# Optimization experiments

Hardware: AMD Instinct MI355X
Metric: run time of the kernel (lower is better)

Reference implementation:

```python
import jax, jax.numpy as jnp
import numpy as np

H = 1024       # hiddenDim
MAXLEN = 512   # maxLen (encoder length)
VOCAB = 32000  # outDim (global in original source)


def setup_inputs() -> dict:
    key = jax.random.key(0)
    ks = jax.random.split(key, 12)
    s = 1.0 / np.sqrt(H)
    u = lambda k, shape: jax.random.uniform(k, shape, jnp.float32, -s, s)
    return {
        "inputId": jax.random.randint(ks[0], (1,), 0, VOCAB),
        "hidden": jax.random.normal(ks[1], (1, 1, H), jnp.float32),
        "encoderOuts": jax.random.normal(ks[2], (MAXLEN, H), jnp.float32),
        "embed_table": jax.random.normal(ks[3], (VOCAB, H), jnp.float32),
        "attn_w": u(ks[4], (MAXLEN, 2 * H)),
        "attn_b": u(ks[5], (MAXLEN,)),
        "comb_w": u(ks[6], (H, 2 * H)),
        "comb_b": u(ks[7], (H,)),
        "w_ih": u(ks[8], (3 * H, H)),
        "w_hh": u(ks[9], (3 * H, H)),
        "b_ih": u(ks[10], (3 * H,)),
        "b_hh": u(ks[11], (3 * H,)),
    }


def reference(inputId, hidden, encoderOuts, embed_table, attn_w, attn_b,
              comb_w, comb_b, w_ih, w_hh, b_ih, b_hh):
    # embedding + (eval-mode) dropout -> identity
    embed = embed_table[inputId].reshape(1, 1, -1)            # (1,1,H)
    # attention over encoder outputs
    cat = jnp.concatenate([embed[0], hidden[0]], axis=1)      # (1,2H)
    attnWeights = jax.nn.softmax(cat @ attn_w.T + attn_b, axis=1)  # (1,MAXLEN)
    attnApplied = attnWeights @ encoderOuts                   # (1,H) == bmm squeeze
    # combine + relu
    x = jnp.concatenate([embed[0], attnApplied], axis=1)      # (1,2H)
    x = jax.nn.relu(x @ comb_w.T + comb_b)                    # (1,H)
    # single GRU step; original calls self.rnn(out) with NO hidden -> h0 = zeros
    h0 = jnp.zeros_like(x)
    gi = x @ w_ih.T + b_ih                                    # (1,3H)
    gh = h0 @ w_hh.T + b_hh                                   # (1,3H)
    i_r, i_z, i_n = jnp.split(gi, 3, axis=1)
    h_r, h_z, h_n = jnp.split(gh, 3, axis=1)
    r = jax.nn.sigmoid(i_r + h_r)
    z = jax.nn.sigmoid(i_z + h_z)
    n = jnp.tanh(i_n + r * h_n)
    h_new = (1.0 - z) * n + z * h0                            # (1,H)
    out = jax.nn.sigmoid(h_new)[None]                         # (1,1,H)
    return out, h_new[None], attnWeights
```

## Files before the change

kernel.cpp:

```cpp
#include <hip/hip_runtime.h>
#include <hip/hip_bf16.h>

#define H 1024
#define MAXLEN 512

typedef __bf16 bf16x8 __attribute__((ext_vector_type(8)));
typedef __bf16 bf16x4 __attribute__((ext_vector_type(4)));
typedef float  f32x4  __attribute__((ext_vector_type(4)));

__device__ __forceinline__ float wave_reduce_sum(float a) {
    #pragma unroll
    for (int off = 32; off; off >>= 1) a += __shfl_xor(a, off);
    return a;
}
__device__ __forceinline__ float wave_reduce_max(float a) {
    #pragma unroll
    for (int off = 32; off; off >>= 1) a = fmaxf(a, __shfl_xor(a, off));
    return a;
}

#define WS_LOGITS 0
#define WS_X      512
#define WS_Y1     2048
#define WS_GT     4096
#define GT_HALF   (1024 * 512)
#define WS_FLOATS (4096 + 2 * GT_HALF)

__global__ __launch_bounds__(512)
void node1(const int* __restrict__ inputId,
           const float* __restrict__ hidden,
           const float* __restrict__ enc,
           const float* __restrict__ embed_table,
           const float* __restrict__ attn_w,
           const float* __restrict__ attn_b,
           const float* __restrict__ comb_w,
           const float* __restrict__ comb_b,
           float* __restrict__ ws) {
    float* logits = ws + WS_LOGITS;
    float* y1     = ws + WS_Y1;

    __shared__ __bf16 Asm[2][128][64];
    __shared__ __bf16 Bsm[2][64][64];

    const int tid  = threadIdx.x;
    const int lane = tid & 63;
    const int w    = tid >> 6;
    const int b    = blockIdx.x;

    if (b < 128) {
        const int pBase = (b & 7) * 128;
        const int qBase = ((b >> 3) & 7) * 64;
        const int kh    = b >> 6;
        const int kBase = kh * 512;
        float* GtH = ws + WS_GT + (size_t)kh * GT_HALF;

        const int wp = w >> 1;
        const int wq = w & 1;
        const int row16 = tid >> 4, c4 = tid & 15;

        f32x4 acc[2][2];
        #pragma unroll
        for (int m = 0; m < 2; ++m)
            #pragma unroll
            for (int n = 0; n < 2; ++n) acc[m][n] = (f32x4){0.f, 0.f, 0.f, 0.f};

        float4 ra[4], rb[2];
        auto loadChunk = [&](int c) {
            const int k0 = kBase + c * 64;
            #pragma unroll
            for (int i = 0; i < 4; ++i)
                ra[i] = *(const float4*)(comb_w + (size_t)(pBase + row16 + i * 32) * 2048 + 1024 + k0 + c4 * 4);
            #pragma unroll
            for (int i = 0; i < 2; ++i)
                rb[i] = *(const float4*)(enc + (size_t)(qBase + row16 + i * 32) * 1024 + k0 + c4 * 4);
        };
        auto writeChunk = [&](int buf) {
            #pragma unroll
            for (int i = 0; i < 4; ++i) {
                int row = row16 + i * 32;
                int off = ((((c4 >> 1) ^ (row & 7)) << 4) | ((c4 & 1) << 3));
                bf16x4 v;
                v[0] = (__bf16)ra[i].x; v[1] = (__bf16)ra[i].y;
                v[2] = (__bf16)ra[i].z; v[3] = (__bf16)ra[i].w;
                *(bf16x4*)((char*)(&Asm[buf][row][0]) + off) = v;
            }
            #pragma unroll
            for (int i = 0; i < 2; ++i) {
                int row = row16 + i * 32;
                int off = ((((c4 >> 1) ^ (row & 7)) << 4) | ((c4 & 1) << 3));
                bf16x4 v;
                v[0] = (__bf16)rb[i].x; v[1] = (__bf16)rb[i].y;
                v[2] = (__bf16)rb[i].z; v[3] = (__bf16)rb[i].w;
                *(bf16x4*)((char*)(&Bsm[buf][row][0]) + off) = v;
            }
        };

        loadChunk(0);
        writeChunk(0);
        __syncthreads();

        for (int c = 0; c < 8; ++c) {
            const int cur = c & 1;
            if (c < 7) loadChunk(c + 1);
            #pragma unroll
            for (int ks = 0; ks < 2; ++ks) {
                const int slot = ks * 4 + (lane >> 4);
                bf16x8 af[2], bfv[2];
                #pragma unroll
                for (int m = 0; m < 2; ++m) {
                    int row = wp * 32 + m * 16 + (lane & 15);
                    af[m] = *(const bf16x8*)((const char*)(&Asm[cur][row][0]) + ((slot ^ (row & 7)) << 4));
                }
                #pragma unroll
                for (int n = 0; n < 2; ++n) {
                    int row = wq * 32 + n * 16 + (lane & 15);
                    bfv[n] = *(const bf16x8*)((const char*)(&Bsm[cur][row][0]) + ((slot ^ (row & 7)) << 4));
                }
                #pragma unroll
                for (int m = 0; m < 2; ++m)
                    #pragma unroll
                    for (int n = 0; n < 2; ++n)
                        acc[m][n] = __builtin_amdgcn_mfma_f32_16x16x32_bf16(af[m], bfv[n], acc[m][n], 0, 0, 0);
            }
            if (c < 7) writeChunk(cur ^ 1);
            __syncthreads();
        }

        #pragma unroll
        for (int m = 0; m < 2; ++m) {
            int p0 = pBase + wp * 32 + m * 16 + (lane >> 4) * 4;
            #pragma unroll
            for (int n = 0; n < 2; ++n) {
                int q = qBase + wq * 32 + n * 16 + (lane & 15);
                #pragma unroll
                for (int i = 0; i < 4; ++i)
                    GtH[(size_t)(p0 + i) * 512 + q] = acc[m][n][i];
            }
        }
    } else if (b < 192) {
        const float* embed = embed_table + (size_t)inputId[0] * H;
        int row = (b - 128) * 8 + w;
        const float* wrow = attn_w + (size_t)row * (2 * H);
        float acc = 0.f;
        #pragma unroll
        for (int it = 0; it < 8; ++it) {
            int base = it * 256 + lane * 4;
            float4 wv = *(const float4*)(wrow + base);
            float4 cv = (it < 4) ? *(const float4*)(embed + base)
                                 : *(const float4*)(hidden + (base - H));
            acc += wv.x * cv.x + wv.y * cv.y + wv.z * cv.z + wv.w * cv.w;
        }
        acc = wave_reduce_sum(acc);
        if (lane == 0) logits[row] = acc + attn_b[row];
    } else {
        const float* embed = embed_table + (size_t)inputId[0] * H;
        #pragma unroll
        for (int rr = 0; rr < 2; ++rr) {
            int row = (b - 192) * 16 + w * 2 + rr;
            const float* wrow = comb_w + (size_t)row * (2 * H);
            float acc = 0.f;
            #pragma unroll
            for (int it = 0; it < 4; ++it) {
                int base = it * 256 + lane * 4;
                float4 wv = *(const float4*)(wrow + base);
                float4 evv = *(const float4*)(embed + base);
                acc += wv.x * evv.x + wv.y * evv.y + wv.z * evv.z + wv.w * evv.w;
            }
            acc = wave_reduce_sum(acc);
            if (lane == 0) y1[row] = acc + comb_b[row];
        }
    }
}

__global__ __launch_bounds__(256)
void node2(float* __restrict__ ws, float* __restrict__ d_out) {
    const float* logits = ws + WS_LOGITS;
    const float* y1     = ws + WS_Y1;
    const float* Gt0    = ws + WS_GT;
    const float* Gt1    = ws + WS_GT + GT_HALF;
    float* x = ws + WS_X;

    __shared__ float wsm[MAXLEN];
    __shared__ float red[4];
    const int tid = threadIdx.x, lane = tid & 63, wid = tid >> 6;
    const int b = blockIdx.x;

    float l0 = logits[tid], l1 = logits[tid + 256];
    float m = wave_reduce_max(fmaxf(l0, l1));
    if (lane == 0) red[wid] = m;
    __syncthreads();
    m = fmaxf(fmaxf(red[0], red[1]), fmaxf(red[2], red[3]));
    __syncthreads();
    float e0 = expf(l0 - m), e1 = expf(l1 - m);
    float s = wave_reduce_sum(e0 + e1);
    if (lane == 0) red[wid] = s;
    __syncthreads();
    s = red[0] + red[1] + red[2] + red[3];
    float inv = 1.f / s;
    float w0 = e0 * inv, w1 = e1 * inv;
    wsm[tid] = w0;
    wsm[tid + 256] = w1;
    if (b == 0) {
        d_out[2048 + tid] = w0;
        d_out[2048 + 256 + tid] = w1;
    }
    __syncthreads();

    #pragma unroll
    for (int rr = 0; rr < 2; ++rr) {
        int row = b * 8 + wid * 2 + rr;
        const float* g0 = Gt0 + (size_t)row * 512;
        const float* g1 = Gt1 + (size_t)row * 512;
        float acc = 0.f;
        #pragma unroll
        for (int i = 0; i < 8; ++i) {
            int k = lane + 64 * i;
            acc += (g0[k] + g1[k]) * wsm[k];
        }
        acc = wave_reduce_sum(acc);
        if (lane == 0) x[row] = fmaxf(y1[row] + acc, 0.f);
    }
}

__global__ __launch_bounds__(256)
void node3(const float* __restrict__ w_ih,
           const float* __restrict__ b_ih,
           const float* __restrict__ b_hh,
           const float* __restrict__ ws,
           float* __restrict__ d_out) {
    const float* x = ws + WS_X;
    int lane = threadIdx.x & 63;
    int j = blockIdx.x * 4 + (threadIdx.x >> 6);
    float acc0 = 0.f, acc1 = 0.f, acc2 = 0.f;
    const float* wr = w_ih + (size_t)j * H;
    const float* wz = w_ih + (size_t)(H + j) * H;
    const float* wn = w_ih + (size_t)(2 * H + j) * H;
    #pragma unroll
    for (int it = 0; it < 4; ++it) {
        int base = it * 256 + lane * 4;
        float4 xv = *(const float4*)(x + base);
        float4 a = *(const float4*)(wr + base);
        float4 c = *(const float4*)(wz + base);
        float4 d = *(const float4*)(wn + base);
        acc0 += a.x * xv.x + a.y * xv.y + a.z * xv.z + a.w * xv.w;
        acc1 += c.x * xv.x + c.y * xv.y + c.z * xv.z + c.w * xv.w;
        acc2 += d.x * xv.x + d.y * xv.y + d.z * xv.z + d.w * xv.w;
    }
    #pragma unroll
    for (int off = 32; off; off >>= 1) {
        acc0 += __shfl_xor(acc0, off);
        acc1 += __shfl_xor(acc1, off);
        acc2 += __shfl_xor(acc2, off);
    }
    if (lane == 0) {
        float gi_r = acc0 + b_ih[j];
        float gi_z = acc1 + b_ih[H + j];
        float gi_n = acc2 + b_ih[2 * H + j];
        float r = 1.f / (1.f + expf(-(gi_r + b_hh[j])));
        float zz = 1.f / (1.f + expf(-(gi_z + b_hh[H + j])));
        float n = tanhf(gi_n + r * b_hh[2 * H + j]);
        float hnew = (1.f - zz) * n;
        float outv = 1.f / (1.f + expf(-hnew));
        d_out[j] = outv;
        d_out[H + j] = hnew;
    }
}

__global__ void fb_kA(const int* __restrict__ inputId, const float* __restrict__ embed_table,
                      const float* __restrict__ hidden, const float* __restrict__ attn_w,
                      const float* __restrict__ attn_b, float* __restrict__ logits) {
    int lane = threadIdx.x & 63;
    int row = blockIdx.x * 4 + (threadIdx.x >> 6);
    const float* embed = embed_table + (size_t)inputId[0] * H;
    const float* wrow = attn_w + (size_t)row * (2 * H);
    float acc = 0.f;
    #pragma unroll
    for (int it = 0; it < 8; ++it) {
        int base = it * 256 + lane * 4;
        float4 wv = *(const float4*)(wrow + base);
        float4 cv = (it < 4) ? *(const float4*)(embed + base)
                             : *(const float4*)(hidden + (base - H));
        acc += wv.x * cv.x + wv.y * cv.y + wv.z * cv.z + wv.w * cv.w;
    }
    acc = wave_reduce_sum(acc);
    if (lane == 0) logits[row] = acc + attn_b[row];
}
__global__ void fb_kB(const float* __restrict__ logits, const float* __restrict__ enc,
                      float* __restrict__ attnApplied, float* __restrict__ out_w) {
    __shared__ float w_lds[MAXLEN];
    __shared__ float red[4];
    __shared__ float part[8][32];
    int tid = threadIdx.x, lane = tid & 63, wid = tid >> 6;
    float l0 = logits[tid], l1 = logits[tid + 256];
    float m = wave_reduce_max(fmaxf(l0, l1));
    if (lane == 0) red[wid] = m;
    __syncthreads();
    m = fmaxf(fmaxf(red[0], red[1]), fmaxf(red[2], red[3]));
    __syncthreads();
    float e0 = expf(l0 - m), e1 = expf(l1 - m);
    float s = wave_reduce_sum(e0 + e1);
    if (lane == 0) red[wid] = s;
    __syncthreads();
    s = red[0] + red[1] + red[2] + red[3];
    float inv = 1.f / s;
    float w0 = e0 * inv, w1 = e1 * inv;
    w_lds[tid] = w0; w_lds[tid + 256] = w1;
    if (blockIdx.x == 0) { out_w[tid] = w0; out_w[tid + 256] = w1; }
    __syncthreads();
    int c = tid & 31, ks = tid >> 5;
    int col = blockIdx.x * 32 + c;
    float acc = 0.f;
    for (int k = ks; k < MAXLEN; k += 8) acc += w_lds[k] * enc[(size_t)k * H + col];
    part[ks][c] = acc;
    __syncthreads();
    if (tid < 32) {
        float t = 0.f;
        #pragma unroll
        for (int i = 0; i < 8; ++i) t += part[i][tid];
        attnApplied[blockIdx.x * 32 + tid] = t;
    }
}
__global__ void fb_kC(const int* __restrict__ inputId, const float* __restrict__ embed_table,
                      const float* __restrict__ attnApplied, const float* __restrict__ comb_w,
                      const float* __restrict__ comb_b, float* __restrict__ x) {
    int lane = threadIdx.x & 63;
    int row = blockIdx.x * 4 + (threadIdx.x >> 6);
    const float* embed = embed_table + (size_t)inputId[0] * H;
    const float* wrow = comb_w + (size_t)row * (2 * H);
    float acc = 0.f;
    #pragma unroll
    for (int it = 0; it < 8; ++it) {
        int base = it * 256 + lane * 4;
        float4 wv = *(const float4*)(wrow + base);
        float4 cv = (it < 4) ? *(const float4*)(embed + base)
                             : *(const float4*)(attnApplied + (base - H));
        acc += wv.x * cv.x + wv.y * cv.y + wv.z * cv.z + wv.w * cv.w;
    }
    acc = wave_reduce_sum(acc);
    if (lane == 0) x[row] = fmaxf(acc + comb_b[row], 0.f);
}
__global__ void fb_kD(const float* __restrict__ w_ih, const float* __restrict__ b_ih,
                      const float* __restrict__ b_hh, const float* __restrict__ x,
                      float* __restrict__ d_out) {
    int lane = threadIdx.x & 63;
    int j = blockIdx.x * 4 + (threadIdx.x >> 6);
    float acc0 = 0.f, acc1 = 0.f, acc2 = 0.f;
    const float* wr = w_ih + (size_t)j * H;
    const float* wz = w_ih + (size_t)(H + j) * H;
    const float* wn = w_ih + (size_t)(2 * H + j) * H;
    #pragma unroll
    for (int it = 0; it < 4; ++it) {
        int base = it * 256 + lane * 4;
        float4 xv = *(const float4*)(x + base);
        float4 a = *(const float4*)(wr + base);
        float4 c = *(const float4*)(wz + base);
        float4 d = *(const float4*)(wn + base);
        acc0 += a.x * xv.x + a.y * xv.y + a.z * xv.z + a.w * xv.w;
        acc1 += c.x * xv.x + c.y * xv.y + c.z * xv.z + c.w * xv.w;
        acc2 += d.x * xv.x + d.y * xv.y + d.z * xv.z + d.w * xv.w;
    }
    #pragma unroll
    for (int off = 32; off; off >>= 1) {
        acc0 += __shfl_xor(acc0, off);
        acc1 += __shfl_xor(acc1, off);
        acc2 += __shfl_xor(acc2, off);
    }
    if (lane == 0) {
        float gi_r = acc0 + b_ih[j];
        float gi_z = acc1 + b_ih[H + j];
        float gi_n = acc2 + b_ih[2 * H + j];
        float r = 1.f / (1.f + expf(-(gi_r + b_hh[j])));
        float z = 1.f / (1.f + expf(-(gi_z + b_hh[H + j])));
        float n = tanhf(gi_n + r * b_hh[2 * H + j]);
        float hnew = (1.f - z) * n;
        float outv = 1.f / (1.f + expf(-hnew));
        d_out[j] = outv;
        d_out[H + j] = hnew;
    }
}

extern "C" void kernel_launch(void* const* d_in, const int* in_sizes, int n_in,
                              void* d_out, int out_size, void* d_ws, size_t ws_size,
                              hipStream_t stream) {
    const int*   inputId     = (const int*)d_in[0];
    const float* hidden      = (const float*)d_in[1];
    const float* enc         = (const float*)d_in[2];
    const float* embed_table = (const float*)d_in[3];
    const float* attn_w      = (const float*)d_in[4];
    const float* attn_b      = (const float*)d_in[5];
    const float* comb_w      = (const float*)d_in[6];
    const float* comb_b      = (const float*)d_in[7];
    const float* w_ih        = (const float*)d_in[8];
    const float* b_ih        = (const float*)d_in[10];
    const float* b_hh        = (const float*)d_in[11];

    float* out = (float*)d_out;
    float* ws  = (float*)d_ws;

    if (ws_size >= (size_t)WS_FLOATS * sizeof(float)) {
        node1<<<256, 512, 0, stream>>>(inputId, hidden, enc, embed_table,
                                       attn_w, attn_b, comb_w, comb_b, ws);
        node2<<<128, 256, 0, stream>>>(ws, out);
        node3<<<256, 256, 0, stream>>>(w_ih, b_ih, b_hh, ws, out);
    } else {
        float* logits      = ws;
        float* attnApplied = ws + 512;
        float* x           = ws + 2048;
        fb_kA<<<128, 256, 0, stream>>>(inputId, embed_table, hidden, attn_w, attn_b, logits);
        fb_kB<<<32,  256, 0, stream>>>(logits, enc, attnApplied, out + 2048);
        fb_kC<<<256, 256, 0, stream>>>(inputId, embed_table, attnApplied, comb_w, comb_b, x);
        fb_kD<<<256, 256, 0, stream>>>(w_ih, b_ih, b_hh, x, out);
    }
}
```

Measured before the change: 24.71 us.

## Fuse attention-apply and GRU input projection into one kernel with split-K atomics

Merges node2 and node3 into one kernel. Each block computes 16 elements of x and then does a split-K partial product of w_ih against those 16 inputs, accumulating into padded gi slots with atomicAdd. A two-level arrival counter picks the last block, which applies the GRU gate math and writes the outputs. node1 zeroes the gi buffer and the counters. This removes a kernel launch and the global round trip of x, at the cost of 3072x128 atomics and a serial tail run by a single block.

```diff
diff --git a/kernel.cpp b/kernel.cpp
--- a/kernel.cpp
+++ b/kernel.cpp
@@ -18,13 +18,17 @@
     for (int off = 32; off; off >>= 1) a = fmaxf(a, __shfl_xor(a, off));
     return a;
 }
+__device__ __forceinline__ float cohLoad(const float* p) {
+    return __hip_atomic_load(p, __ATOMIC_RELAXED, __HIP_MEMORY_SCOPE_AGENT);
+}
 
 #define WS_LOGITS 0
-#define WS_X      512
-#define WS_Y1     2048
+#define WS_Y1     512
+#define WS_CNT    1536
 #define WS_GT     4096
 #define GT_HALF   (1024 * 512)
-#define WS_FLOATS (4096 + 2 * GT_HALF)
+#define WS_GI     (WS_GT + 2 * GT_HALF)
+#define WS_FLOATS (WS_GI + 3072 * 16)
 
 __global__ __launch_bounds__(512)
 void node1(const int* __restrict__ inputId,
@@ -169,48 +173,64 @@
             acc = wave_reduce_sum(acc);
             if (lane == 0) y1[row] = acc + comb_b[row];
         }
-    }
-}
-
-__global__ __launch_bounds__(256)
-void node2(float* __restrict__ ws, float* __restrict__ d_out) {
+        if (b < 200) {
+            float* gi = ws + WS_GI;
+            int bz = b - 192;
+            #pragma unroll
+            for (int q = 0; q < 12; ++q)
+                gi[bz * 6144 + q * 512 + tid] = 0.f;
+            if (b == 192 && tid < 9)
+                *(unsigned*)(ws + WS_CNT + tid * 16) = 0u;
+        }
+    }
+}
+
+__global__ __launch_bounds__(512)
+void node2(const float* __restrict__ w_ih,
+           const float* __restrict__ b_ih,
+           const float* __restrict__ b_hh,
+           float* __restrict__ ws,
+           float* __restrict__ d_out) {
     const float* logits = ws + WS_LOGITS;
     const float* y1     = ws + WS_Y1;
     const float* Gt0    = ws + WS_GT;
     const float* Gt1    = ws + WS_GT + GT_HALF;
-    float* x = ws + WS_X;
+    float* gi = ws + WS_GI;
+    unsigned* cnt = (unsigned*)(ws + WS_CNT);
 
     __shared__ float wsm[MAXLEN];
-    __shared__ float red[4];
-    const int tid = threadIdx.x, lane = tid & 63, wid = tid >> 6;
+    __shared__ float redm[8], reds[8];
+    __shared__ float x_lds[16];
+    __shared__ int lastFlag;
+
+    const int tid = threadIdx.x, lane = tid & 63, w = tid >> 6;
     const int b = blockIdx.x;
-
-    float l0 = logits[tid], l1 = logits[tid + 256];
-    float m = wave_reduce_max(fmaxf(l0, l1));
-    if (lane == 0) red[wid] = m;
-    __syncthreads();
-    m = fmaxf(fmaxf(red[0], red[1]), fmaxf(red[2], red[3]));
-    __syncthreads();
-    float e0 = expf(l0 - m), e1 = expf(l1 - m);
-    float s = wave_reduce_sum(e0 + e1);
-    if (lane == 0) red[wid] = s;
-    __syncthreads();
-    s = red[0] + red[1] + red[2] + red[3];
-    float inv = 1.f / s;
-    float w0 = e0 * inv, w1 = e1 * inv;
-    wsm[tid] = w0;
-    wsm[tid + 256] = w1;
-    if (b == 0) {
-        d_out[2048 + tid] = w0;
-        d_out[2048 + 256 + tid] = w1;
-    }
+    const int g = b >> 6, b16 = b & 63;
+
+    float l = logits[tid];
+    float m = wave_reduce_max(l);
+    if (lane == 0) redm[w] = m;
+    __syncthreads();
+    m = redm[0];
+    #pragma unroll
+    for (int i = 1; i < 8; ++i) m = fmaxf(m, redm[i]);
+    float e = expf(l - m);
+    float s = wave_reduce_sum(e);
+    if (lane == 0) reds[w] = s;
+    __syncthreads();
+    s = 0.f;
+    #pragma unroll
+    for (int i = 0; i < 8; ++i) s += reds[i];
+    float wgt = e / s;
+    wsm[tid] = wgt;
+    if (b == 0) d_out[2048 + tid] = wgt;
     __syncthreads();
 
     #pragma unroll
     for (int rr = 0; rr < 2; ++rr) {
-        int row = b * 8 + wid * 2 + rr;
-        const float* g0 = Gt0 + (size_t)row * 512;
-        const float* g1 = Gt1 + (size_t)row * 512;
+        int r = b16 * 16 + w * 2 + rr;
+        const float* g0 = Gt0 + (size_t)r * 512;
+        const float* g1 = Gt1 + (size_t)r * 512;
         float acc = 0.f;
         #pragma unroll
         for (int i = 0; i < 8; ++i) {
@@ -218,51 +238,60 @@
             acc += (g0[k] + g1[k]) * wsm[k];
         }
         acc = wave_reduce_sum(acc);
-        if (lane == 0) x[row] = fmaxf(y1[row] + acc, 0.f);
-    }
-}
-
-__global__ __launch_bounds__(256)
-void node3(const float* __restrict__ w_ih,
-           const float* __restrict__ b_ih,
-           const float* __restrict__ b_hh,
-           const float* __restrict__ ws,
-           float* __restrict__ d_out) {
-    const float* x = ws + WS_X;
-    int lane = threadIdx.x & 63;
-    int j = blockIdx.x * 4 + (threadIdx.x >> 6);
-    float acc0 = 0.f, acc1 = 0.f, acc2 = 0.f;
-    const float* wr = w_ih + (size_t)j * H;
-    const float* wz = w_ih + (size_t)(H + j) * H;
-    const float* wn = w_ih + (size_t)(2 * H + j) * H;
-    #pragma unroll
-    for (int it = 0; it < 4; ++it) {
-        int base = it * 256 + lane * 4;
-        float4 xv = *(const float4*)(x + base);
-        float4 a = *(const float4*)(wr + base);
-        float4 c = *(const float4*)(wz + base);
-        float4 d = *(const float4*)(wn + base);
-        acc0 += a.x * xv.x + a.y * xv.y + a.z * xv.z + a.w * xv.w;
-        acc1 += c.x * xv.x + c.y * xv.y + c.z * xv.z + c.w * xv.w;
-        acc2 += d.x * xv.x + d.y * xv.y + d.z * xv.z + d.w * xv.w;
-    }
-    #pragma unroll
-    for (int off = 32; off; off >>= 1) {
-        acc0 += __shfl_xor(acc0, off);
-        acc1 += __shfl_xor(acc1, off);
-        acc2 += __shfl_xor(acc2, off);
-    }
-    if (lane == 0) {
-        float gi_r = acc0 + b_ih[j];
-        float gi_z = acc1 + b_ih[H + j];
-        float gi_n = acc2 + b_ih[2 * H + j];
-        float r = 1.f / (1.f + expf(-(gi_r + b_hh[j])));
-        float zz = 1.f / (1.f + expf(-(gi_z + b_hh[H + j])));
-        float n = tanhf(gi_n + r * b_hh[2 * H + j]);
-        float hnew = (1.f - zz) * n;
-        float outv = 1.f / (1.f + expf(-hnew));
-        d_out[j] = outv;
-        d_out[H + j] = hnew;
+        if (lane == 0) x_lds[w * 2 + rr] = fmaxf(y1[r] + acc, 0.f);
+    }
+    __syncthreads();
+
+    float xr[16];
+    #pragma unroll
+    for (int kk = 0; kk < 16; ++kk) xr[kk] = x_lds[kk];
+
+    const int k0 = b16 * 16;
+    #pragma unroll
+    for (int ii = 0; ii < 3; ++ii) {
+        int j = g * 1536 + ii * 512 + tid;
+        const float* wr = w_ih + (size_t)j * H + k0;
+        float4 a0 = *(const float4*)(wr);
+        float4 a1 = *(const float4*)(wr + 4);
+        float4 a2 = *(const float4*)(wr + 8);
+        float4 a3 = *(const float4*)(wr + 12);
+        float acc = a0.x * xr[0]  + a0.y * xr[1]  + a0.z * xr[2]  + a0.w * xr[3]
+                  + a1.x * xr[4]  + a1.y * xr[5]  + a1.z * xr[6]  + a1.w * xr[7]
+                  + a2.x * xr[8]  + a2.y * xr[9]  + a2.z * xr[10] + a2.w * xr[11]
+                  + a3.x * xr[12] + a3.y * xr[13] + a3.z * xr[14] + a3.w * xr[15];
+        atomicAdd(gi + (size_t)j * 16, acc);
+    }
+
+    __builtin_amdgcn_fence(__ATOMIC_RELEASE, "agent");
+    if (tid == 0) {
+        lastFlag = 0;
+        unsigned o = __hip_atomic_fetch_add(cnt + (b >> 4) * 16, 1u,
+                                            __ATOMIC_ACQ_REL, __HIP_MEMORY_SCOPE_AGENT);
+        if (o == 15u) {
+            unsigned r2 = __hip_atomic_fetch_add(cnt + 128, 1u,
+                                                 __ATOMIC_ACQ_REL, __HIP_MEMORY_SCOPE_AGENT);
+            if (r2 == 7u) lastFlag = 1;
+        }
+    }
+    __syncthreads();
+
+    if (lastFlag) {
+        __builtin_amdgcn_fence(__ATOMIC_ACQUIRE, "agent");
+        for (int jj = tid; jj < 1024; jj += 512) {
+            float gr = cohLoad(gi + (size_t)jj * 16);
+            float gz = cohLoad(gi + (size_t)(1024 + jj) * 16);
+            float gn = cohLoad(gi + (size_t)(2048 + jj) * 16);
+            float gi_r = gr + b_ih[jj];
+            float gi_z = gz + b_ih[1024 + jj];
+            float gi_n = gn + b_ih[2048 + jj];
+            float r = 1.f / (1.f + expf(-(gi_r + b_hh[jj])));
+            float z = 1.f / (1.f + expf(-(gi_z + b_hh[1024 + jj])));
+            float n = tanhf(gi_n + r * b_hh[2048 + jj]);
+            float hnew = (1.f - z) * n;
+            float outv = 1.f / (1.f + expf(-hnew));
+            d_out[jj] = outv;
+            d_out[1024 + jj] = hnew;
+        }
     }
 }
 
@@ -400,8 +429,7 @@
     if (ws_size >= (size_t)WS_FLOATS * sizeof(float)) {
         node1<<<256, 512, 0, stream>>>(inputId, hidden, enc, embed_table,
                                        attn_w, attn_b, comb_w, comb_b, ws);
-        node2<<<128, 256, 0, stream>>>(ws, out);
-        node3<<<256, 256, 0, stream>>>(w_ih, b_ih, b_hh, ws, out);
+        node2<<<128, 512, 0, stream>>>(w_ih, b_ih, b_hh, ws, out);
     } else {
         float* logits      = ws;
         float* attnApplied = ws + 512;
```

Result: slower. 51.96 us (+110.3%).
